# Performance work log

Hardware: AMD Instinct MI355X
Metric: run time of the kernel (lower is better)

Reference implementation:

```python
import jax, jax.numpy as jnp
import numpy as np

HID = 128
NEG = 9000000000000000.0  # 9e15 additive mask constant from the source


def setup_inputs() -> dict:
    key = jax.random.key(0)
    ks = jax.random.split(key, 20)
    B, N, OBS, N1, N2 = 32, 2048, 256, 8, 8
    x = jax.random.normal(ks[0], (B, N, OBS), dtype=jnp.float32)
    mask = jax.random.randint(ks[1], (B, N, N), 0, 2).astype(jnp.float32)

    def lin(kw, kb, fan_in, fan_out):
        bound = 1.0 / np.sqrt(fan_in)
        W = jax.random.uniform(kw, (fan_in, fan_out), jnp.float32, -bound, bound)
        b = jax.random.uniform(kb, (fan_out,), jnp.float32, -bound, bound)
        return W, b

    Wv, bv = lin(ks[2], ks[3], OBS, HID)
    Wk, bk = lin(ks[4], ks[5], OBS, HID)
    Wq, bq = lin(ks[6], ks[7], OBS, HID)
    Wout, bout = lin(ks[8], ks[9], HID, HID)
    Wval, bval = lin(ks[10], ks[11], HID, 1)
    Wadv1, badv1 = lin(ks[12], ks[13], HID, N1)
    Wadv2, badv2 = lin(ks[14], ks[15], HID, N2)
    return {
        'x': x, 'mask': mask,
        'Wv': Wv, 'bv': bv, 'Wk': Wk, 'bk': bk, 'Wq': Wq, 'bq': bq,
        'Wout': Wout, 'bout': bout, 'Wval': Wval, 'bval': bval,
        'Wadv1': Wadv1, 'badv1': badv1, 'Wadv2': Wadv2, 'badv2': badv2,
    }


def reference(x, mask, Wv, bv, Wk, bk, Wq, bq, Wout, bout,
              Wval, bval, Wadv1, badv1, Wadv2, badv2):
    # AttenModel
    v = jax.nn.relu(x @ Wv + bv)          # [B,N,H]
    q = jax.nn.relu(x @ Wq + bq)          # [B,N,H]
    k = jax.nn.relu(x @ Wk + bk)          # [B,N,H]
    scores = jnp.einsum('bnh,bmh->bnm', q, k)          # [B,N,N]
    scores = scores * mask - NEG * (1.0 - mask)
    att = jax.nn.softmax(scores, axis=2)
    out = jnp.einsum('bnm,bmh->bnh', att, v)            # [B,N,H]
    out = jax.nn.relu(out @ Wout + bout)                # [B,N,H]
    # Dueling heads (batch > 1, so squeeze(0) is a no-op)
    value = out @ Wval + bval                            # [B,N,1]
    adv1 = out @ Wadv1 + badv1                           # [B,N,n1]
    adv2 = out @ Wadv2 + badv2                           # [B,N,n2]
    q1 = value + adv1 - adv1.mean(axis=1, keepdims=True)
    q2 = value + adv2 - adv2.mean(axis=1, keepdims=True)
    return (q1, q2)
```

## Files before the change

kernel.cpp:

```cpp
#include <hip/hip_runtime.h>
#include <hip/hip_bf16.h>


typedef __attribute__((ext_vector_type(4))) float f32x4;
typedef __attribute__((ext_vector_type(8))) short bf16x8;
typedef __attribute__((ext_vector_type(4))) unsigned int u32x4;

#define LOG2E 1.44269504088896340736f
#define NEGC 9.0e15f

static __device__ __forceinline__ unsigned short f2bf(float f) {
  unsigned int x = __builtin_bit_cast(unsigned int, f);
  unsigned int r = (x + 0x7fffu + ((x >> 16) & 1u)) >> 16;
  return (unsigned short)r;
}
static __device__ __forceinline__ float bf2f(unsigned short u) {
  return __builtin_bit_cast(float, ((unsigned int)u) << 16);
}
static __device__ __forceinline__ unsigned int pack2bf(float lo, float hi) {
  return (unsigned int)f2bf(lo) | ((unsigned int)f2bf(hi) << 16);
}
static __device__ __forceinline__ f32x4 mfma16(bf16x8 a, bf16x8 b, f32x4 c) {
  return __builtin_amdgcn_mfma_f32_16x16x32_bf16(a, b, c, 0, 0, 0);
}

__global__ __launch_bounds__(256) void prep_kernel(
    const float* __restrict__ Wv, const float* __restrict__ Wk,
    const float* __restrict__ Wq, const float* __restrict__ Wout,
    unsigned short* __restrict__ Wf_hi, unsigned short* __restrict__ Wf_lo,
    unsigned short* __restrict__ WoutT) {
  int gid = blockIdx.x * 256 + threadIdx.x;
  if (gid < 12288) {
    int kc = gid / 1536;
    int rem = gid - kc * 1536;
    int t = rem >> 6, lane = rem & 63;
    int hf = lane & 15, qf = lane >> 4;
    int sec = t >> 3;
    int j = (t & 7) * 16 + hf;
    const float* W = (sec == 0) ? Wq : (sec == 1) ? Wk : Wv;
#pragma unroll
    for (int e = 0; e < 8; ++e) {
      int k = kc * 32 + qf * 8 + e;
      float w = W[k * 128 + j];
      unsigned short hi = f2bf(w);
      Wf_hi[gid * 8 + e] = hi;
      Wf_lo[gid * 8 + e] = f2bf(w - bf2f(hi));
    }
  } else if (gid < 12288 + 16384) {
    int i2 = gid - 12288;
    int j = i2 >> 7, c = i2 & 127;
    WoutT[i2] = f2bf(Wout[c * 128 + j]);
  }
}

__global__ __launch_bounds__(256, 2) void fused_pp_kernel(
    const float* __restrict__ x,
    const unsigned short* __restrict__ Wf_hi, const unsigned short* __restrict__ Wf_lo,
    const float* __restrict__ bq, const float* __restrict__ bk, const float* __restrict__ bv,
    unsigned short* __restrict__ q_bf, unsigned short* __restrict__ Kf,
    unsigned short* __restrict__ Vf,
    const float* __restrict__ mask, unsigned long long* __restrict__ bits) {
  __shared__ bf16x8 wst_hi[1536];
  __shared__ bf16x8 wst_lo[1536];
  __shared__ unsigned short vbuf[9216];

  const int tid = threadIdx.x;
  const int lane = tid & 63, wid = tid >> 6;
  const int bid = blockIdx.x;
  const int role = bid % 3;

  if (role != 0) {
    const int pidx = (bid / 3) * 2 + (role - 1);
    const int gwave = pidx * 4 + wid;
    const int T = lane & 3;
    const int sh = T << 4;
    for (int r = 0; r < 8; ++r) {
      const long row = (long)gwave * 8 + r;
      const float* mp = mask + row * 2048;
      unsigned long long* op = bits + row * 32;
#pragma unroll
      for (int g = 0; g < 8; ++g) {
        f32x4 v = *(const f32x4*)(mp + g * 256 + lane * 4);
        unsigned long long b0 = __ballot(v[0] != 0.0f);
        unsigned long long b1 = __ballot(v[1] != 0.0f);
        unsigned long long b2 = __ballot(v[2] != 0.0f);
        unsigned long long b3 = __ballot(v[3] != 0.0f);
        unsigned long long f0 = (b0 >> sh) & 0xFFFFull;
        unsigned long long f1 = (b1 >> sh) & 0xFFFFull;
        unsigned long long f2 = (b2 >> sh) & 0xFFFFull;
        unsigned long long f3 = (b3 >> sh) & 0xFFFFull;
        unsigned long long val = f0 | (f1 << 16) | (f2 << 32) | (f3 << 48);
        if (lane < 4) op[g * 4 + T] = val;
      }
    }
    return;
  }

  const int pb = bid / 3;
  const long rbase = (long)pb * 64;
  const int qq = lane >> 4, hh = lane & 15;
  const long rowA = rbase + wid * 16 + hh;
  const f32x4 zero4 = {0.f, 0.f, 0.f, 0.f};
  f32x4 acc[24];
#pragma unroll
  for (int t = 0; t < 24; ++t) acc[t] = zero4;

  for (int kc = 0; kc < 8; ++kc) {
    __syncthreads();
#pragma unroll
    for (int i = 0; i < 6; ++i) {
      int idx = i * 256 + tid;
      wst_hi[idx] = *(const bf16x8*)(Wf_hi + ((long)kc * 1536 + idx) * 8);
      wst_lo[idx] = *(const bf16x8*)(Wf_lo + ((long)kc * 1536 + idx) * 8);
    }
    __syncthreads();

    const float* xp = x + rowA * 256 + kc * 32 + qq * 8;
    f32x4 x0 = *(const f32x4*)xp;
    f32x4 x1 = *(const f32x4*)(xp + 4);
    bf16x8 ah, al;
#pragma unroll
    for (int j = 0; j < 8; ++j) {
      float f = (j < 4) ? x0[j] : x1[j - 4];
      unsigned short h = f2bf(f);
      ah[j] = (short)h;
      al[j] = (short)f2bf(f - bf2f(h));
    }
#pragma unroll
    for (int t = 0; t < 24; ++t) {
      bf16x8 bh = wst_hi[t * 64 + lane];
      bf16x8 bl = wst_lo[t * 64 + lane];
      acc[t] = mfma16(ah, bh, acc[t]);
      acc[t] = mfma16(al, bh, acc[t]);
      acc[t] = mfma16(ah, bl, acc[t]);
    }
  }

  const int rowL = wid * 16 + qq * 4;
  const int b = (int)(rbase >> 11);
  const int tbase = (int)((rbase & 2047) >> 6);

  for (int sec = 0; sec < 3; ++sec) {
    __syncthreads();
#pragma unroll
    for (int tp = 0; tp < 8; ++tp) {
      const int t = sec * 8 + tp;
      const int j = tp * 16 + hh;
      const float bias = (sec == 0) ? bq[j] : (sec == 1) ? bk[j] : bv[j];
#pragma unroll
      for (int r = 0; r < 4; ++r) {
        unsigned short h = f2bf(fmaxf(acc[t][r] + bias, 0.f));
        if (sec == 2) vbuf[j * 72 + rowL + r] = h;
        else          vbuf[(rowL + r) * 136 + j] = h;
      }
    }
    __syncthreads();
    if (sec == 0) {
      const int row = tid >> 2, ch = tid & 3;
      bf16x8 w1 = *(const bf16x8*)&vbuf[row * 136 + ch * 32];
      bf16x8 w2 = *(const bf16x8*)&vbuf[row * 136 + ch * 32 + 8];
      bf16x8 w3 = *(const bf16x8*)&vbuf[row * 136 + ch * 32 + 16];
      bf16x8 w4 = *(const bf16x8*)&vbuf[row * 136 + ch * 32 + 24];
      unsigned short* op = q_bf + (rbase + row) * 128 + ch * 32;
      *(bf16x8*)op = w1;
      *(bf16x8*)(op + 8) = w2;
      *(bf16x8*)(op + 16) = w3;
      *(bf16x8*)(op + 24) = w4;
    } else if (sec == 1) {
#pragma unroll
      for (int it = 0; it < 4; ++it) {
        int gid = it * 256 + tid;
        int seg = gid >> 6, ln = gid & 63;
        int m = seg >> 2, kc = seg & 3;
        int hf = ln & 15, qf = ln >> 4;
        bf16x8 w = *(const bf16x8*)&vbuf[(m * 16 + hf) * 136 + kc * 32 + qf * 8];
        long off = (((long)(b * 32 + tbase) * 16 + seg) * 64 + ln) * 8;
        *(bf16x8*)(Kf + off) = w;
      }
    } else {
#pragma unroll
      for (int it = 0; it < 4; ++it) {
        int gid = it * 256 + tid;
        int seg = gid >> 6, ln = gid & 63;
        int ht = seg >> 1, c = seg & 1;
        int hf = ln & 15, qf = ln >> 4;
        bf16x8 w = *(const bf16x8*)&vbuf[(ht * 16 + hf) * 72 + c * 32 + qf * 8];
        long off = (((long)(b * 32 + tbase) * 16 + seg) * 64 + ln) * 8;
        *(bf16x8*)(Vf + off) = w;
      }
    }
  }
}

__global__ __launch_bounds__(256, 2) void attn_kernel(
    const unsigned short* __restrict__ q_bf, const unsigned short* __restrict__ Kf,
    const unsigned short* __restrict__ Vf,
    const unsigned long long* __restrict__ bits, unsigned short* __restrict__ out_att) {
  __shared__ bf16x8 kls[2][1024];
  __shared__ bf16x8 vls[2][1024];

  const int tid = threadIdx.x;
  const int lane = tid & 63, wid = tid >> 6;
  const int qq = lane >> 4, hh = lane & 15;
  const int orig = blockIdx.x;
  const int b = ((orig & 7) << 2) | ((orig >> 3) & 3);
  const int nb = orig >> 5;
  const long qbase = (long)b * 2048 + nb * 128 + wid * 32;

  const f32x4 zero4 = {0.f, 0.f, 0.f, 0.f};

  bf16x8 qh[2][4];
#pragma unroll
  for (int ctq = 0; ctq < 2; ++ctq)
#pragma unroll
    for (int kc = 0; kc < 4; ++kc)
      qh[ctq][kc] = *(const bf16x8*)(q_bf + (qbase + ctq * 16 + hh) * 128 + kc * 32 + qq * 8);

  const unsigned long long* br0 = bits + (qbase + hh) * 32;
  const unsigned long long* br1 = bits + (qbase + 16 + hh) * 32;
  const unsigned short* kf0 = Kf + (long)(b * 32) * 8192;
  const unsigned short* vf0 = Vf + (long)(b * 32) * 8192;

  f32x4 o_acc[8][2];
#pragma unroll
  for (int ht = 0; ht < 8; ++ht) { o_acc[ht][0] = zero4; o_acc[ht][1] = zero4; }
  float m_run[2] = {-3.0e38f, -3.0e38f};
  float l_run[2] = {0.f, 0.f};

  bf16x8 stg[8];
  const int seg0 = wid * 8;
  auto LOADREG = [&](int t) {
#pragma unroll
    for (int i = 0; i < 8; ++i) {
      int seg = seg0 + i;
      const unsigned short* src = (seg < 16)
          ? kf0 + (long)t * 8192 + (seg * 64 + lane) * 8
          : vf0 + (long)t * 8192 + ((seg - 16) * 64 + lane) * 8;
      stg[i] = *(const bf16x8*)src;
    }
  };
  auto WRITEBUF = [&](int nb2) {
#pragma unroll
    for (int i = 0; i < 8; ++i) {
      int seg = seg0 + i;
      if (seg < 16) kls[nb2][seg * 64 + lane] = stg[i];
      else          vls[nb2][(seg - 16) * 64 + lane] = stg[i];
    }
  };

  LOADREG(0);
  WRITEBUF(0);
  LOADREG(1);
  __syncthreads();

  unsigned long long bc0 = br0[0];
  unsigned long long bc1 = br1[0];

  const int src0 = (((qq << 1)) & 3) * 16 + hh;
  const int src1 = (((qq << 1) + 1) & 3) * 16 + hh;
  const bool hiq = qq >= 2;
  int cur = 0;

  for (int t = 0; t < 32; ++t) {
    unsigned long long bn0 = 0, bn1 = 0;
    if (t + 1 < 32) { bn0 = br0[t + 1]; bn1 = br1[t + 1]; }

    if (t + 1 < 32) WRITEBUF(cur ^ 1);
    if (t + 2 < 32) LOADREG(t + 2);

    f32x4 s[2][4];
#pragma unroll
    for (int m = 0; m < 4; ++m) { s[0][m] = zero4; s[1][m] = zero4; }
    __builtin_amdgcn_s_setprio(1);
#pragma unroll
    for (int m = 0; m < 4; ++m) {
      bf16x8 khf[4];
#pragma unroll
      for (int kc = 0; kc < 4; ++kc) khf[kc] = kls[cur][(m * 4 + kc) * 64 + lane];
#pragma unroll
      for (int kc = 0; kc < 4; ++kc)
#pragma unroll
        for (int ctq = 0; ctq < 2; ++ctq)
          s[ctq][m] = mfma16(khf[kc], qh[ctq][kc], s[ctq][m]);
    }
    __builtin_amdgcn_s_setprio(0);

    {
      const unsigned long long bb0 = bc0 >> qq;
      const unsigned long long bb1 = bc1 >> qq;
#pragma unroll
      for (int m = 0; m < 4; ++m)
#pragma unroll
        for (int r = 0; r < 4; ++r) {
          const int sh = r * 16 + m * 4;
          s[0][m][r] = ((bb0 >> sh) & 1ull) ? s[0][m][r] : -NEGC;
          s[1][m][r] = ((bb1 >> sh) & 1ull) ? s[1][m][r] : -NEGC;
        }
    }

    unsigned int pk[2][4][2];
#pragma unroll
    for (int ctq = 0; ctq < 2; ++ctq) {
      float mx = s[ctq][0][0];
#pragma unroll
      for (int m = 0; m < 4; ++m)
#pragma unroll
        for (int r = 0; r < 4; ++r) mx = fmaxf(mx, s[ctq][m][r]);
      mx = fmaxf(mx, __shfl_xor(mx, 16, 64));
      mx = fmaxf(mx, __shfl_xor(mx, 32, 64));
      if (__any(mx > m_run[ctq] + 8.0f)) {
        float mnew = fmaxf(m_run[ctq], mx);
        float sc = exp2f((m_run[ctq] - mnew) * LOG2E);
        m_run[ctq] = mnew;
        l_run[ctq] *= sc;
#pragma unroll
        for (int ht = 0; ht < 8; ++ht) o_acc[ht][ctq] *= sc;
      }
      float ps = 0.f;
#pragma unroll
      for (int m = 0; m < 4; ++m)
#pragma unroll
        for (int r = 0; r < 4; ++r) {
          float p = exp2f((s[ctq][m][r] - m_run[ctq]) * LOG2E);
          s[ctq][m][r] = p;
          ps += p;
        }
      ps += __shfl_xor(ps, 16, 64);
      ps += __shfl_xor(ps, 32, 64);
      l_run[ctq] += ps;
#pragma unroll
      for (int m = 0; m < 4; ++m) {
        pk[ctq][m][0] = pack2bf(s[ctq][m][0], s[ctq][m][1]);
        pk[ctq][m][1] = pack2bf(s[ctq][m][2], s[ctq][m][3]);
      }
    }

    bf16x8 pb[2][2];
#pragma unroll
    for (int ctq = 0; ctq < 2; ++ctq)
#pragma unroll
      for (int c = 0; c < 2; ++c) {
        unsigned int a0 = (unsigned int)__shfl((int)pk[ctq][2 * c][0], src0, 64);
        unsigned int a1 = (unsigned int)__shfl((int)pk[ctq][2 * c][1], src0, 64);
        unsigned int a2 = (unsigned int)__shfl((int)pk[ctq][2 * c][0], src1, 64);
        unsigned int a3 = (unsigned int)__shfl((int)pk[ctq][2 * c][1], src1, 64);
        unsigned int b0 = (unsigned int)__shfl((int)pk[ctq][2 * c + 1][0], src0, 64);
        unsigned int b1 = (unsigned int)__shfl((int)pk[ctq][2 * c + 1][1], src0, 64);
        unsigned int b2 = (unsigned int)__shfl((int)pk[ctq][2 * c + 1][0], src1, 64);
        unsigned int b3 = (unsigned int)__shfl((int)pk[ctq][2 * c + 1][1], src1, 64);
        u32x4 w;
        w[0] = hiq ? b0 : a0;
        w[1] = hiq ? b1 : a1;
        w[2] = hiq ? b2 : a2;
        w[3] = hiq ? b3 : a3;
        pb[ctq][c] = __builtin_bit_cast(bf16x8, w);
      }

    __builtin_amdgcn_s_setprio(1);
#pragma unroll
    for (int ht = 0; ht < 8; ++ht)
#pragma unroll
      for (int c = 0; c < 2; ++c) {
        bf16x8 vf = vls[cur][(ht * 2 + c) * 64 + lane];
#pragma unroll
        for (int ctq = 0; ctq < 2; ++ctq)
          o_acc[ht][ctq] = mfma16(vf, pb[ctq][c], o_acc[ht][ctq]);
      }
    __builtin_amdgcn_s_setprio(0);

    __syncthreads();
    cur ^= 1;
    bc0 = bn0;
    bc1 = bn1;
  }

#pragma unroll
  for (int ctq = 0; ctq < 2; ++ctq) {
    float inv = 1.0f / l_run[ctq];
    const long row = qbase + ctq * 16 + hh;
#pragma unroll
    for (int ht = 0; ht < 8; ++ht) {
      f32x4 o = o_acc[ht][ctq];
      uint2 w;
      w.x = pack2bf(o[0] * inv, o[1] * inv);
      w.y = pack2bf(o[2] * inv, o[3] * inv);
      *(uint2*)(out_att + row * 128 + ht * 16 + qq * 4) = w;
    }
  }
}

__global__ __launch_bounds__(256) void wout_heads_kernel(
    const unsigned short* __restrict__ out_att, const unsigned short* __restrict__ WoutT,
    const float* __restrict__ bout,
    const float* __restrict__ Wval, const float* __restrict__ bval,
    const float* __restrict__ Wadv1, const float* __restrict__ badv1,
    const float* __restrict__ Wadv2, const float* __restrict__ badv2,
    float* __restrict__ value, float* __restrict__ adv1, float* __restrict__ adv2) {
  const int lane = threadIdx.x & 63, wid = threadIdx.x >> 6;
  const int qq = lane >> 4, hh = lane & 15;
  const long rowA = (long)blockIdx.x * 64 + wid * 16 + hh;
  const f32x4 zero4 = {0.f, 0.f, 0.f, 0.f};
  f32x4 acc[8];
#pragma unroll
  for (int t = 0; t < 8; ++t) acc[t] = zero4;
#pragma unroll
  for (int kc = 0; kc < 4; ++kc) {
    bf16x8 af = *(const bf16x8*)(out_att + rowA * 128 + kc * 32 + qq * 8);
#pragma unroll
    for (int t = 0; t < 8; ++t) {
      bf16x8 bf = *(const bf16x8*)(WoutT + (t * 16 + hh) * 128 + kc * 32 + qq * 8);
      acc[t] = mfma16(af, bf, acc[t]);
    }
  }
  float pv[4] = {0.f, 0.f, 0.f, 0.f};
  float pa1[4][8], pa2[4][8];
#pragma unroll
  for (int r = 0; r < 4; ++r)
#pragma unroll
    for (int j = 0; j < 8; ++j) { pa1[r][j] = 0.f; pa2[r][j] = 0.f; }
#pragma unroll
  for (int t = 0; t < 8; ++t) {
    const int col = t * 16 + hh;
    const float bo = bout[col];
    const float wv = Wval[col];
    const f32x4 w1a = *(const f32x4*)(Wadv1 + col * 8);
    const f32x4 w1b = *(const f32x4*)(Wadv1 + col * 8 + 4);
    const f32x4 w2a = *(const f32x4*)(Wadv2 + col * 8);
    const f32x4 w2b = *(const f32x4*)(Wadv2 + col * 8 + 4);
#pragma unroll
    for (int r = 0; r < 4; ++r) {
      float h = fmaxf(acc[t][r] + bo, 0.f);
      pv[r] += h * wv;
#pragma unroll
      for (int j = 0; j < 4; ++j) {
        pa1[r][j]     += h * w1a[j];
        pa1[r][4 + j] += h * w1b[j];
        pa2[r][j]     += h * w2a[j];
        pa2[r][4 + j] += h * w2b[j];
      }
    }
  }
#pragma unroll
  for (int r = 0; r < 4; ++r) {
#pragma unroll
    for (int s = 1; s < 16; s <<= 1) {
      pv[r] += __shfl_xor(pv[r], s, 64);
#pragma unroll
      for (int j = 0; j < 8; ++j) {
        pa1[r][j] += __shfl_xor(pa1[r][j], s, 64);
        pa2[r][j] += __shfl_xor(pa2[r][j], s, 64);
      }
    }
  }
  if (hh == 0) {
    const float bv0 = bval[0];
#pragma unroll
    for (int r = 0; r < 4; ++r) {
      const long row = (long)blockIdx.x * 64 + wid * 16 + qq * 4 + r;
      value[row] = pv[r] + bv0;
#pragma unroll
      for (int j = 0; j < 8; ++j) {
        adv1[row * 8 + j] = pa1[r][j] + badv1[j];
        adv2[row * 8 + j] = pa2[r][j] + badv2[j];
      }
    }
  }
}

__global__ __launch_bounds__(256) void sums_kernel(const float* __restrict__ adv1,
                                                   const float* __restrict__ adv2,
                                                   float* __restrict__ sums) {
  const int b = blockIdx.x, tid = threadIdx.x;
  __shared__ float red[4][16];
  float p[16];
#pragma unroll
  for (int j = 0; j < 16; ++j) p[j] = 0.f;
  for (int n = tid; n < 2048; n += 256) {
    const long row = (long)b * 2048 + n;
    const f32x4 a1a = *(const f32x4*)(adv1 + row * 8);
    const f32x4 a1b = *(const f32x4*)(adv1 + row * 8 + 4);
    const f32x4 a2a = *(const f32x4*)(adv2 + row * 8);
    const f32x4 a2b = *(const f32x4*)(adv2 + row * 8 + 4);
#pragma unroll
    for (int j = 0; j < 4; ++j) {
      p[j] += a1a[j]; p[4 + j] += a1b[j];
      p[8 + j] += a2a[j]; p[12 + j] += a2b[j];
    }
  }
#pragma unroll
  for (int s = 1; s < 64; s <<= 1)
#pragma unroll
    for (int j = 0; j < 16; ++j) p[j] += __shfl_xor(p[j], s, 64);
  const int wid = tid >> 6;
  if ((tid & 63) == 0)
#pragma unroll
    for (int j = 0; j < 16; ++j) red[wid][j] = p[j];
  __syncthreads();
  if (tid < 16)
    sums[b * 16 + tid] = red[0][tid] + red[1][tid] + red[2][tid] + red[3][tid];
}

__global__ void combine_kernel(const float* __restrict__ value, const float* __restrict__ adv1,
                               const float* __restrict__ adv2, const float* __restrict__ sums,
                               float* __restrict__ out) {
  const int idx = blockIdx.x * 256 + threadIdx.x;
  const int half = 524288;
  const int which = (idx >= half) ? 1 : 0;
  const int rem = idx - which * half;
  const int b = rem >> 14;
  const int r2 = rem & 16383;
  const int n = r2 >> 3, j = r2 & 7;
  const long row = (long)b * 2048 + n;
  const float* adv = which ? adv2 : adv1;
  const float mean = sums[b * 16 + which * 8 + j] * (1.0f / 2048.0f);
  out[idx] = value[row] + adv[row * 8 + j] - mean;
}

extern "C" void kernel_launch(void* const* d_in, const int* in_sizes, int n_in,
                              void* d_out, int out_size, void* d_ws, size_t ws_size,
                              hipStream_t stream) {
  const float* x     = (const float*)d_in[0];
  const float* mask  = (const float*)d_in[1];
  const float* Wv    = (const float*)d_in[2];
  const float* bv    = (const float*)d_in[3];
  const float* Wk    = (const float*)d_in[4];
  const float* bk    = (const float*)d_in[5];
  const float* Wq    = (const float*)d_in[6];
  const float* bq    = (const float*)d_in[7];
  const float* Wout  = (const float*)d_in[8];
  const float* bout  = (const float*)d_in[9];
  const float* Wval  = (const float*)d_in[10];
  const float* bval  = (const float*)d_in[11];
  const float* Wadv1 = (const float*)d_in[12];
  const float* badv1 = (const float*)d_in[13];
  const float* Wadv2 = (const float*)d_in[14];
  const float* badv2 = (const float*)d_in[15];
  float* out = (float*)d_out;
  char* ws = (char*)d_ws;

  unsigned short* q_bf   = (unsigned short*)(ws + 0);
  unsigned short* Kf     = (unsigned short*)(ws + 16777216);
  unsigned short* Vf     = (unsigned short*)(ws + 33554432);
  unsigned short* out_at = (unsigned short*)(ws + 50331648);
  float* value = (float*)(ws + 67108864);
  float* adv1  = (float*)(ws + 67371008);
  float* adv2  = (float*)(ws + 69468160);
  float* sums  = (float*)(ws + 71565312);
  unsigned short* Wf_hi = (unsigned short*)(ws + 71567360);
  unsigned short* Wf_lo = (unsigned short*)(ws + 71763968);
  unsigned short* WoutT = (unsigned short*)(ws + 71960576);
  unsigned long long* bits = (unsigned long long*)(ws + 71993344);

  prep_kernel<<<112, 256, 0, stream>>>(Wv, Wk, Wq, Wout, Wf_hi, Wf_lo, WoutT);
  fused_pp_kernel<<<3072, 256, 0, stream>>>(x, Wf_hi, Wf_lo, bq, bk, bv,
                                            q_bf, Kf, Vf, mask, bits);
  attn_kernel<<<512, 256, 0, stream>>>(q_bf, Kf, Vf, bits, out_at);
  wout_heads_kernel<<<1024, 256, 0, stream>>>(out_at, WoutT, bout, Wval, bval,
                                              Wadv1, badv1, Wadv2, badv2,
                                              value, adv1, adv2);
  sums_kernel<<<32, 256, 0, stream>>>(adv1, adv2, sums);
  combine_kernel<<<4096, 256, 0, stream>>>(value, adv1, adv2, sums, out);
}
```

Baseline: 400.6 us.

## Split mask packing into its own kernel and use permlane swaps for P

Undoes the role-split fusion of mask bit-packing with the QKV projection, launching a separate prepack kernel and a projection-only kernel. Inside the attention loop, the eight ds_bpermute-style shuffles plus selects that rearranged packed P fragments are replaced by v_permlane32_swap/v_permlane16_swap instructions, which exchange registers across lane halves without going through LDS. The split loses the overlap between the bandwidth-bound mask pass and the compute-bound projection, and adds one kernel launch. The permlane swap sequence has to reproduce exactly the lane mapping the old shuffles used.

```diff
diff --git a/kernel.cpp b/kernel.cpp
--- a/kernel.cpp
+++ b/kernel.cpp
@@ -22,6 +22,33 @@
 }
 static __device__ __forceinline__ f32x4 mfma16(bf16x8 a, bf16x8 b, f32x4 c) {
   return __builtin_amdgcn_mfma_f32_16x16x32_bf16(a, b, c, 0, 0, 0);
+}
+
+__global__ __launch_bounds__(256) void prepack_kernel(const float* __restrict__ mask,
+                                                      unsigned long long* __restrict__ bits) {
+  const int lane = threadIdx.x & 63;
+  const int gwave = (blockIdx.x << 2) | (threadIdx.x >> 6);
+  const int T = lane & 3;
+  const int sh = T << 4;
+  for (int r = 0; r < 8; ++r) {
+    const long row = (long)gwave * 8 + r;
+    const float* mp = mask + row * 2048;
+    unsigned long long* op = bits + row * 32;
+#pragma unroll
+    for (int g = 0; g < 8; ++g) {
+      f32x4 v = *(const f32x4*)(mp + g * 256 + lane * 4);
+      unsigned long long b0 = __ballot(v[0] != 0.0f);
+      unsigned long long b1 = __ballot(v[1] != 0.0f);
+      unsigned long long b2 = __ballot(v[2] != 0.0f);
+      unsigned long long b3 = __ballot(v[3] != 0.0f);
+      unsigned long long f0 = (b0 >> sh) & 0xFFFFull;
+      unsigned long long f1 = (b1 >> sh) & 0xFFFFull;
+      unsigned long long f2 = (b2 >> sh) & 0xFFFFull;
+      unsigned long long f3 = (b3 >> sh) & 0xFFFFull;
+      unsigned long long val = f0 | (f1 << 16) | (f2 << 32) | (f3 << 48);
+      if (lane < 4) op[g * 4 + T] = val;
+    }
+  }
 }
 
 __global__ __launch_bounds__(256) void prep_kernel(
@@ -53,51 +80,19 @@
   }
 }
 
-__global__ __launch_bounds__(256, 2) void fused_pp_kernel(
+__global__ __launch_bounds__(256, 2) void proj_kernel(
     const float* __restrict__ x,
     const unsigned short* __restrict__ Wf_hi, const unsigned short* __restrict__ Wf_lo,
     const float* __restrict__ bq, const float* __restrict__ bk, const float* __restrict__ bv,
     unsigned short* __restrict__ q_bf, unsigned short* __restrict__ Kf,
-    unsigned short* __restrict__ Vf,
-    const float* __restrict__ mask, unsigned long long* __restrict__ bits) {
+    unsigned short* __restrict__ Vf) {
   __shared__ bf16x8 wst_hi[1536];
   __shared__ bf16x8 wst_lo[1536];
   __shared__ unsigned short vbuf[9216];
 
   const int tid = threadIdx.x;
   const int lane = tid & 63, wid = tid >> 6;
-  const int bid = blockIdx.x;
-  const int role = bid % 3;
-
-  if (role != 0) {
-    const int pidx = (bid / 3) * 2 + (role - 1);
-    const int gwave = pidx * 4 + wid;
-    const int T = lane & 3;
-    const int sh = T << 4;
-    for (int r = 0; r < 8; ++r) {
-      const long row = (long)gwave * 8 + r;
-      const float* mp = mask + row * 2048;
-      unsigned long long* op = bits + row * 32;
-#pragma unroll
-      for (int g = 0; g < 8; ++g) {
-        f32x4 v = *(const f32x4*)(mp + g * 256 + lane * 4);
-        unsigned long long b0 = __ballot(v[0] != 0.0f);
-        unsigned long long b1 = __ballot(v[1] != 0.0f);
-        unsigned long long b2 = __ballot(v[2] != 0.0f);
-        unsigned long long b3 = __ballot(v[3] != 0.0f);
-        unsigned long long f0 = (b0 >> sh) & 0xFFFFull;
-        unsigned long long f1 = (b1 >> sh) & 0xFFFFull;
-        unsigned long long f2 = (b2 >> sh) & 0xFFFFull;
-        unsigned long long f3 = (b3 >> sh) & 0xFFFFull;
-        unsigned long long val = f0 | (f1 << 16) | (f2 << 32) | (f3 << 48);
-        if (lane < 4) op[g * 4 + T] = val;
-      }
-    }
-    return;
-  }
-
-  const int pb = bid / 3;
-  const long rbase = (long)pb * 64;
+  const long rbase = (long)blockIdx.x * 64;
   const int qq = lane >> 4, hh = lane & 15;
   const long rowA = rbase + wid * 16 + hh;
   const f32x4 zero4 = {0.f, 0.f, 0.f, 0.f};
@@ -255,10 +250,6 @@
 
   unsigned long long bc0 = br0[0];
   unsigned long long bc1 = br1[0];
-
-  const int src0 = (((qq << 1)) & 3) * 16 + hh;
-  const int src1 = (((qq << 1) + 1) & 3) * 16 + hh;
-  const bool hiq = qq >= 2;
   int cur = 0;
 
   for (int t = 0; t < 32; ++t) {
@@ -340,19 +331,16 @@
     for (int ctq = 0; ctq < 2; ++ctq)
 #pragma unroll
       for (int c = 0; c < 2; ++c) {
-        unsigned int a0 = (unsigned int)__shfl((int)pk[ctq][2 * c][0], src0, 64);
-        unsigned int a1 = (unsigned int)__shfl((int)pk[ctq][2 * c][1], src0, 64);
-        unsigned int a2 = (unsigned int)__shfl((int)pk[ctq][2 * c][0], src1, 64);
-        unsigned int a3 = (unsigned int)__shfl((int)pk[ctq][2 * c][1], src1, 64);
-        unsigned int b0 = (unsigned int)__shfl((int)pk[ctq][2 * c + 1][0], src0, 64);
-        unsigned int b1 = (unsigned int)__shfl((int)pk[ctq][2 * c + 1][1], src0, 64);
-        unsigned int b2 = (unsigned int)__shfl((int)pk[ctq][2 * c + 1][0], src1, 64);
-        unsigned int b3 = (unsigned int)__shfl((int)pk[ctq][2 * c + 1][1], src1, 64);
+        unsigned int a  = pk[ctq][2 * c][0];
+        unsigned int bb = pk[ctq][2 * c][1];
+        unsigned int cc = pk[ctq][2 * c + 1][0];
+        unsigned int d  = pk[ctq][2 * c + 1][1];
+        asm("v_permlane32_swap_b32 %0, %1" : "+v"(a),  "+v"(cc));
+        asm("v_permlane32_swap_b32 %0, %1" : "+v"(bb), "+v"(d));
+        asm("v_permlane16_swap_b32 %0, %1" : "+v"(a),  "+v"(cc));
+        asm("v_permlane16_swap_b32 %0, %1" : "+v"(bb), "+v"(d));
         u32x4 w;
-        w[0] = hiq ? b0 : a0;
-        w[1] = hiq ? b1 : a1;
-        w[2] = hiq ? b2 : a2;
-        w[3] = hiq ? b3 : a3;
+        w[0] = a; w[1] = bb; w[2] = cc; w[3] = d;
         pb[ctq][c] = __builtin_bit_cast(bf16x8, w);
       }
 
@@ -551,9 +539,9 @@
   unsigned short* WoutT = (unsigned short*)(ws + 71960576);
   unsigned long long* bits = (unsigned long long*)(ws + 71993344);
 
+  prepack_kernel<<<2048, 256, 0, stream>>>(mask, bits);
   prep_kernel<<<112, 256, 0, stream>>>(Wv, Wk, Wq, Wout, Wf_hi, Wf_lo, WoutT);
-  fused_pp_kernel<<<3072, 256, 0, stream>>>(x, Wf_hi, Wf_lo, bq, bk, bv,
-                                            q_bf, Kf, Vf, mask, bits);
+  proj_kernel<<<1024, 256, 0, stream>>>(x, Wf_hi, Wf_lo, bq, bk, bv, q_bf, Kf, Vf);
   attn_kernel<<<512, 256, 0, stream>>>(q_bf, Kf, Vf, bits, out_at);
   wout_heads_kernel<<<1024, 256, 0, stream>>>(out_at, WoutT, bout, Wval, bval,
                                               Wadv1, badv1, Wadv2, badv2,
```

Measured after the change: 335.5 us. 16.2% less time.
